# Kernel tuning notes

Measured on AMD Instinct MI355X. Metric: run time of the kernel, lower is better.

The kernel has to match this reference:

```python
import jax, jax.numpy as jnp
import numpy as np

B, T, C, HS = 256, 256, 384, 64

def setup_inputs() -> dict:
    key = jax.random.key(0)
    k1, k2, k3, k4 = jax.random.split(key, 4)
    s = 1.0 / np.sqrt(C)  # Linear-like init scale
    return {
        "x": jax.random.normal(k1, (B, T, C), dtype=jnp.float32),
        "Wq": jax.random.normal(k2, (C, HS), dtype=jnp.float32) * s,
        "Wk": jax.random.normal(k3, (C, HS), dtype=jnp.float32) * s,
        "Wv": jax.random.normal(k4, (C, HS), dtype=jnp.float32) * s,
    }

def reference(x, Wq, Wk, Wv):
    # q,k,v: [B,T,HS]
    q = jnp.einsum("btc,ch->bth", x, Wq)
    k = jnp.einsum("btc,ch->bth", x, Wk)
    v = jnp.einsum("btc,ch->bth", x, Wv)
    scale = k.shape[-1] ** -0.5
    scores = jnp.einsum("bth,bsh->bts", q, k) * scale  # [B,T,T]
    causal = jnp.tril(jnp.ones((x.shape[1], x.shape[1]), dtype=bool))
    scores = jnp.where(causal, scores, -jnp.inf)
    attn = jax.nn.softmax(scores, axis=-1)
    # dropout omitted (eval mode / deterministic reference)
    return jnp.einsum("bts,bsh->bth", attn, v)
```

## Files before the change

kernel.cpp:

```cpp
#include <hip/hip_runtime.h>
#include <hip/hip_bf16.h>

#define NB 256
#define NT 256
#define NC 384
#define NH 64
#define NW 192
#define WT_ELEMS (NW * NC)

typedef short bf16x8 __attribute__((ext_vector_type(8)));
typedef float f32x4 __attribute__((ext_vector_type(4)));

__device__ __forceinline__ unsigned short f2bf(float f) {
  union { float f; unsigned int i; } c;
  c.f = f;
  const unsigned int r = c.i + 0x7fffu + ((c.i >> 16) & 1u);
  return (unsigned short)(r >> 16);
}

__device__ __forceinline__ unsigned short f2bf_hw(float f) {
  __hip_bfloat16 b = __float2bfloat16(f);
  return *reinterpret_cast<unsigned short*>(&b);
}

__device__ __forceinline__ bf16x8 cvt8(float4 lo, float4 hi) {
  union { bf16x8 v; unsigned short u[8]; } au;
  au.u[0] = f2bf_hw(lo.x); au.u[1] = f2bf_hw(lo.y);
  au.u[2] = f2bf_hw(lo.z); au.u[3] = f2bf_hw(lo.w);
  au.u[4] = f2bf_hw(hi.x); au.u[5] = f2bf_hw(hi.y);
  au.u[6] = f2bf_hw(hi.z); au.u[7] = f2bf_hw(hi.w);
  return au.v;
}

__global__ __launch_bounds__(256) void w_prep_kernel(
    const float* __restrict__ Wq,
    const float* __restrict__ Wk,
    const float* __restrict__ Wv,
    unsigned short* __restrict__ Wt2) {
  const int o = blockIdx.x * 256 + threadIdx.x;
  if (o >= WT_ELEMS) return;
  const int j = o & 7;
  const int lane = (o >> 3) & 63;
  const int fi = o >> 9;
  const int ni = fi % 12;
  const int kt = fi / 12;
  const int n = ni * 16 + (lane & 15);
  const int k = kt * 32 + ((lane >> 4) << 3) + j;
  const float* W = (n < 64) ? Wq : (n < 128) ? Wk : Wv;
  Wt2[o] = f2bf(W[k * NH + (n & 63)]);
}

__global__ __launch_bounds__(512, 2) void fused_qkv_attn_kernel(
    const float* __restrict__ x,
    const unsigned short* __restrict__ Wt2,
    float* __restrict__ out) {
  __shared__ __align__(16) unsigned char lds[118784];

  const int tid = threadIdx.x;
  const int w = tid >> 6;
  const int lane = tid & 63;
  const int l15 = lane & 15;
  const int lg = lane >> 4;
  const int b = blockIdx.x;
  const int row0 = b * NT;
  const int qt = (w < 4) ? w : 11 - w;
  const int wbase = qt * 32;

  f32x4 acc[2][12];
#pragma unroll
  for (int mi = 0; mi < 2; ++mi)
#pragma unroll
    for (int ni = 0; ni < 12; ++ni)
#pragma unroll
      for (int r = 0; r < 4; ++r) acc[mi][ni][r] = 0.f;

  const float* xa0 = x + (size_t)(row0 + wbase + l15) * NC + lg * 8;
  const float* xa1 = xa0 + (size_t)16 * NC;
  const unsigned short* wfrag = Wt2 + lane * 8;

#pragma unroll 2
  for (int kt = 0; kt < 12; ++kt) {
    const float4 a0lo = *reinterpret_cast<const float4*>(xa0 + kt * 32);
    const float4 a0hi = *reinterpret_cast<const float4*>(xa0 + kt * 32 + 4);
    const float4 a1lo = *reinterpret_cast<const float4*>(xa1 + kt * 32);
    const float4 a1hi = *reinterpret_cast<const float4*>(xa1 + kt * 32 + 4);
    const bf16x8 afr0 = cvt8(a0lo, a0hi);
    const bf16x8 afr1 = cvt8(a1lo, a1hi);
#pragma unroll
    for (int ni = 0; ni < 12; ++ni) {
      const bf16x8 bfr = *reinterpret_cast<const bf16x8*>(
          wfrag + (size_t)(kt * 12 + ni) * 512);
      acc[0][ni] = __builtin_amdgcn_mfma_f32_16x16x32_bf16(
          afr0, bfr, acc[0][ni], 0, 0, 0);
      acc[1][ni] = __builtin_amdgcn_mfma_f32_16x16x32_bf16(
          afr1, bfr, acc[1][ni], 0, 0, 0);
    }
  }

  unsigned short* Kls = reinterpret_cast<unsigned short*>(lds);
  unsigned short* Vtls = reinterpret_cast<unsigned short*>(lds + 32768);
  unsigned short* Qls = reinterpret_cast<unsigned short*>(lds + 65536);
  unsigned short* Pls = reinterpret_cast<unsigned short*>(lds + 98304);

#pragma unroll
  for (int mi = 0; mi < 2; ++mi)
#pragma unroll
    for (int ni = 0; ni < 12; ++ni) {
      const int n = ni * 16 + l15;
#pragma unroll
      for (int r = 0; r < 4; ++r) {
        const int srow = wbase + mi * 16 + lg * 4 + r;
        const unsigned short val = f2bf_hw(acc[mi][ni][r]);
        if (ni < 4) {
          Qls[srow * 64 + (n ^ ((srow & 7) << 3))] = val;
        } else if (ni < 8) {
          const int h = n - 64;
          Kls[srow * 64 + (h ^ ((srow & 7) << 3))] = val;
        } else {
          const int h = n - 128;
          Vtls[h * 256 + (srow ^ ((h & 7) << 3))] = val;
        }
      }
    }
  __syncthreads();

  const int q0 = wbase;
  bf16x8 a_q[2][2];
#pragma unroll
  for (int mi = 0; mi < 2; ++mi)
#pragma unroll
    for (int ks = 0; ks < 2; ++ks) {
      const int srow = q0 + mi * 16 + l15;
      a_q[mi][ks] = *reinterpret_cast<const bf16x8*>(
          Qls + srow * 64 + ((ks * 32 + lg * 8) ^ ((srow & 7) << 3)));
    }

  f32x4 o[2][4];
  float mrun[2][4], lrun[2][4];
#pragma unroll
  for (int mi = 0; mi < 2; ++mi)
#pragma unroll
    for (int r = 0; r < 4; ++r) {
      mrun[mi][r] = -3.0e38f;
      lrun[mi][r] = 0.f;
#pragma unroll
      for (int hi = 0; hi < 4; ++hi) o[mi][hi][r] = 0.f;
    }

  unsigned short* Pw = Pls + w * 1280;

  for (int j = 0; j <= qt; ++j) {
    f32x4 s_acc[2][2];
#pragma unroll
    for (int mi = 0; mi < 2; ++mi)
#pragma unroll
      for (int si = 0; si < 2; ++si)
#pragma unroll
        for (int r = 0; r < 4; ++r) s_acc[mi][si][r] = 0.f;

#pragma unroll
    for (int ks = 0; ks < 2; ++ks) {
      bf16x8 bk[2];
#pragma unroll
      for (int si = 0; si < 2; ++si) {
        const int srow = j * 32 + si * 16 + l15;
        const int kel = ks * 32 + lg * 8;
        bk[si] = *reinterpret_cast<const bf16x8*>(
            Kls + srow * 64 + (kel ^ ((srow & 7) << 3)));
      }
#pragma unroll
      for (int mi = 0; mi < 2; ++mi)
#pragma unroll
        for (int si = 0; si < 2; ++si)
          s_acc[mi][si] = __builtin_amdgcn_mfma_f32_16x16x32_bf16(
              a_q[mi][ks], bk[si], s_acc[mi][si], 0, 0, 0);
    }

    const bool diag = (j == qt);
#pragma unroll
    for (int mi = 0; mi < 2; ++mi) {
#pragma unroll
      for (int r = 0; r < 4; ++r) {
        const int mloc = mi * 16 + lg * 4 + r;
        float v0 = s_acc[mi][0][r] * 0.125f;
        float v1 = s_acc[mi][1][r] * 0.125f;
        if (diag) {
          if (l15 > mloc) v0 = -3.0e38f;
          if (16 + l15 > mloc) v1 = -3.0e38f;
        }
        float pm = fmaxf(v0, v1);
        pm = fmaxf(pm, __shfl_xor(pm, 1, 16));
        pm = fmaxf(pm, __shfl_xor(pm, 2, 16));
        pm = fmaxf(pm, __shfl_xor(pm, 4, 16));
        pm = fmaxf(pm, __shfl_xor(pm, 8, 16));
        const float mnew = fmaxf(mrun[mi][r], pm);
        const float alpha = __expf(mrun[mi][r] - mnew);
        mrun[mi][r] = mnew;
        const float p0 = __expf(v0 - mnew);
        const float p1 = __expf(v1 - mnew);
        float ps = p0 + p1;
        ps += __shfl_xor(ps, 1, 16);
        ps += __shfl_xor(ps, 2, 16);
        ps += __shfl_xor(ps, 4, 16);
        ps += __shfl_xor(ps, 8, 16);
        lrun[mi][r] = lrun[mi][r] * alpha + ps;
#pragma unroll
        for (int hi = 0; hi < 4; ++hi) o[mi][hi][r] *= alpha;
        Pw[mloc * 40 + l15] = f2bf(p0);
        Pw[mloc * 40 + 16 + l15] = f2bf(p1);
      }
    }

    bf16x8 pa[2];
#pragma unroll
    for (int mt = 0; mt < 2; ++mt)
      pa[mt] = *reinterpret_cast<const bf16x8*>(
          Pw + (mt * 16 + l15) * 40 + lg * 8);
#pragma unroll
    for (int hi = 0; hi < 4; ++hi) {
      const int h = hi * 16 + l15;
      const int sel = j * 32 + lg * 8;
      const bf16x8 bv = *reinterpret_cast<const bf16x8*>(
          Vtls + h * 256 + (sel ^ ((h & 7) << 3)));
#pragma unroll
      for (int mt = 0; mt < 2; ++mt)
        o[mt][hi] = __builtin_amdgcn_mfma_f32_16x16x32_bf16(
            pa[mt], bv, o[mt][hi], 0, 0, 0);
    }
  }

  float* og = out + ((size_t)b * NT + q0) * NH;
#pragma unroll
  for (int mi = 0; mi < 2; ++mi)
#pragma unroll
    for (int r = 0; r < 4; ++r) {
      const float inv = 1.f / lrun[mi][r];
      const int m = mi * 16 + lg * 4 + r;
#pragma unroll
      for (int hi = 0; hi < 4; ++hi)
        og[m * 64 + hi * 16 + l15] = o[mi][hi][r] * inv;
    }
}

extern "C" void kernel_launch(void* const* d_in, const int* in_sizes, int n_in,
                              void* d_out, int out_size, void* d_ws,
                              size_t ws_size, hipStream_t stream) {
  const float* x  = (const float*)d_in[0];
  const float* Wq = (const float*)d_in[1];
  const float* Wk = (const float*)d_in[2];
  const float* Wv = (const float*)d_in[3];
  unsigned short* Wt2 = (unsigned short*)d_ws;
  float* out = (float*)d_out;

  w_prep_kernel<<<dim3((WT_ELEMS + 255) / 256), dim3(256), 0, stream>>>(
      Wq, Wk, Wv, Wt2);
  fused_qkv_attn_kernel<<<dim3(NB), dim3(512), 0, stream>>>(x, Wt2, out);
}
```

Measured before the change: 44.94 us.

## Stage packed weights into LDS via async global_load_lds and prefetch x three deep

The whole packed bf16 weight matrix (144 KB) is now copied into LDS at kernel start with global_load_lds, so the QKV projection reads B fragments from LDS instead of re-reading them from global/L2 in every wave. The x row loads are software-pipelined three k-steps ahead with explicit register buffers and a manual vmcnt wait. The larger LDS footprint (147456 bytes) likely allows only one block per CU instead of two, which reduces occupancy and latency hiding. A barrier is added after the projection before the LDS is reused for Q/K/V.

```diff
diff --git a/kernel.cpp b/kernel.cpp
--- a/kernel.cpp
+++ b/kernel.cpp
@@ -54,7 +54,7 @@
     const float* __restrict__ x,
     const unsigned short* __restrict__ Wt2,
     float* __restrict__ out) {
-  __shared__ __align__(16) unsigned char lds[118784];
+  __shared__ __align__(16) unsigned char lds[147456];
 
   const int tid = threadIdx.x;
   const int w = tid >> 6;
@@ -74,28 +74,58 @@
 #pragma unroll
       for (int r = 0; r < 4; ++r) acc[mi][ni][r] = 0.f;
 
+#pragma unroll
+  for (int i = 0; i < 18; ++i) {
+    const int idx = i * 512 + tid;
+    __builtin_amdgcn_global_load_lds(
+        (const __attribute__((address_space(1))) void*)(Wt2 + idx * 8),
+        (__attribute__((address_space(3))) void*)(lds + idx * 16), 16, 0, 0);
+  }
+
   const float* xa0 = x + (size_t)(row0 + wbase + l15) * NC + lg * 8;
   const float* xa1 = xa0 + (size_t)16 * NC;
-  const unsigned short* wfrag = Wt2 + lane * 8;
-
-#pragma unroll 2
-  for (int kt = 0; kt < 12; ++kt) {
-    const float4 a0lo = *reinterpret_cast<const float4*>(xa0 + kt * 32);
-    const float4 a0hi = *reinterpret_cast<const float4*>(xa0 + kt * 32 + 4);
-    const float4 a1lo = *reinterpret_cast<const float4*>(xa1 + kt * 32);
-    const float4 a1hi = *reinterpret_cast<const float4*>(xa1 + kt * 32 + 4);
-    const bf16x8 afr0 = cvt8(a0lo, a0hi);
-    const bf16x8 afr1 = cvt8(a1lo, a1hi);
-#pragma unroll
-    for (int ni = 0; ni < 12; ++ni) {
-      const bf16x8 bfr = *reinterpret_cast<const bf16x8*>(
-          wfrag + (size_t)(kt * 12 + ni) * 512);
-      acc[0][ni] = __builtin_amdgcn_mfma_f32_16x16x32_bf16(
-          afr0, bfr, acc[0][ni], 0, 0, 0);
-      acc[1][ni] = __builtin_amdgcn_mfma_f32_16x16x32_bf16(
-          afr1, bfr, acc[1][ni], 0, 0, 0);
-    }
-  }
+
+  float4 aA0, aA1, aA2, aA3, aB0, aB1, aB2, aB3, aC0, aC1, aC2, aC3;
+
+#define LOADA(S, KT)                                                          \
+  do {                                                                        \
+    a##S##0 = *reinterpret_cast<const float4*>(xa0 + (KT)*32);                \
+    a##S##1 = *reinterpret_cast<const float4*>(xa0 + (KT)*32 + 4);            \
+    a##S##2 = *reinterpret_cast<const float4*>(xa1 + (KT)*32);                \
+    a##S##3 = *reinterpret_cast<const float4*>(xa1 + (KT)*32 + 4);            \
+  } while (0)
+
+  LOADA(A, 0);
+  LOADA(B, 1);
+  LOADA(C, 2);
+
+  asm volatile("s_waitcnt vmcnt(12)" ::: "memory");
+  __builtin_amdgcn_s_barrier();
+
+  const unsigned short* Wl =
+      reinterpret_cast<const unsigned short*>(lds) + lane * 8;
+
+#define STEP(S, KT)                                                           \
+  do {                                                                        \
+    const bf16x8 afr0 = cvt8(a##S##0, a##S##1);                               \
+    const bf16x8 afr1 = cvt8(a##S##2, a##S##3);                               \
+    if ((KT) + 3 < 12) LOADA(S, (KT) + 3);                                    \
+    _Pragma("unroll") for (int ni = 0; ni < 12; ++ni) {                       \
+      const bf16x8 bfr = *reinterpret_cast<const bf16x8*>(                    \
+          Wl + (size_t)((KT)*12 + ni) * 512);                                 \
+      acc[0][ni] = __builtin_amdgcn_mfma_f32_16x16x32_bf16(                   \
+          afr0, bfr, acc[0][ni], 0, 0, 0);                                    \
+      acc[1][ni] = __builtin_amdgcn_mfma_f32_16x16x32_bf16(                   \
+          afr1, bfr, acc[1][ni], 0, 0, 0);                                    \
+    }                                                                         \
+  } while (0)
+
+  STEP(A, 0);  STEP(B, 1);  STEP(C, 2);
+  STEP(A, 3);  STEP(B, 4);  STEP(C, 5);
+  STEP(A, 6);  STEP(B, 7);  STEP(C, 8);
+  STEP(A, 9);  STEP(B, 10); STEP(C, 11);
+
+  __syncthreads();
 
   unsigned short* Kls = reinterpret_cast<unsigned short*>(lds);
   unsigned short* Vtls = reinterpret_cast<unsigned short*>(lds + 32768);
```

New measurement: 44.22 us. No clear change (-1.6%).

## Stage x and weights through LDS with async global_load_lds double buffering

Applied to the files above, without the earlier changes.

Rewrites the QKV projection so weight fragments are copied into LDS in three K-thirds using async global_load_lds with two buffers. x tiles are loaded coalesced, converted to bf16 and stored swizzled into per-wave LDS regions, with manual waitcnt and barriers used to overlap loads with MFMA work. This removes redundant per-wave global weight reads and uncoalesced x loads. In exchange LDS grows to 160KB, which likely limits occupancy to one block per CU, and the hand-written vmcnt counts are fragile.

```diff
diff --git a/kernel.cpp b/kernel.cpp
--- a/kernel.cpp
+++ b/kernel.cpp
@@ -21,15 +21,6 @@
 __device__ __forceinline__ unsigned short f2bf_hw(float f) {
   __hip_bfloat16 b = __float2bfloat16(f);
   return *reinterpret_cast<unsigned short*>(&b);
-}
-
-__device__ __forceinline__ bf16x8 cvt8(float4 lo, float4 hi) {
-  union { bf16x8 v; unsigned short u[8]; } au;
-  au.u[0] = f2bf_hw(lo.x); au.u[1] = f2bf_hw(lo.y);
-  au.u[2] = f2bf_hw(lo.z); au.u[3] = f2bf_hw(lo.w);
-  au.u[4] = f2bf_hw(hi.x); au.u[5] = f2bf_hw(hi.y);
-  au.u[6] = f2bf_hw(hi.z); au.u[7] = f2bf_hw(hi.w);
-  return au.v;
 }
 
 __global__ __launch_bounds__(256) void w_prep_kernel(
@@ -54,7 +45,7 @@
     const float* __restrict__ x,
     const unsigned short* __restrict__ Wt2,
     float* __restrict__ out) {
-  __shared__ __align__(16) unsigned char lds[118784];
+  __shared__ __align__(16) unsigned char lds[163840];
 
   const int tid = threadIdx.x;
   const int w = tid >> 6;
@@ -74,28 +65,89 @@
 #pragma unroll
       for (int r = 0; r < 4; ++r) acc[mi][ni][r] = 0.f;
 
-  const float* xa0 = x + (size_t)(row0 + wbase + l15) * NC + lg * 8;
-  const float* xa1 = xa0 + (size_t)16 * NC;
-  const unsigned short* wfrag = Wt2 + lane * 8;
-
-#pragma unroll 2
-  for (int kt = 0; kt < 12; ++kt) {
-    const float4 a0lo = *reinterpret_cast<const float4*>(xa0 + kt * 32);
-    const float4 a0hi = *reinterpret_cast<const float4*>(xa0 + kt * 32 + 4);
-    const float4 a1lo = *reinterpret_cast<const float4*>(xa1 + kt * 32);
-    const float4 a1hi = *reinterpret_cast<const float4*>(xa1 + kt * 32 + 4);
-    const bf16x8 afr0 = cvt8(a0lo, a0hi);
-    const bf16x8 afr1 = cvt8(a1lo, a1hi);
-#pragma unroll
-    for (int ni = 0; ni < 12; ++ni) {
-      const bf16x8 bfr = *reinterpret_cast<const bf16x8*>(
-          wfrag + (size_t)(kt * 12 + ni) * 512);
-      acc[0][ni] = __builtin_amdgcn_mfma_f32_16x16x32_bf16(
-          afr0, bfr, acc[0][ni], 0, 0, 0);
-      acc[1][ni] = __builtin_amdgcn_mfma_f32_16x16x32_bf16(
-          afr1, bfr, acc[1][ni], 0, 0, 0);
-    }
-  }
+  float4 xr[16];
+
+#define XLOAD(T)                                                              \
+  {                                                                           \
+    _Pragma("unroll") for (int i = 0; i < 16; ++i) {                          \
+      const int idx_ = i * 64 + lane;                                         \
+      const int r_ = idx_ >> 5, c_ = idx_ & 31;                               \
+      xr[i] = *reinterpret_cast<const float4*>(                               \
+          x + (size_t)(row0 + wbase + r_) * NC + (T)*128 + c_ * 4);           \
+    }                                                                         \
+  }
+
+#define XWRITE()                                                              \
+  {                                                                           \
+    _Pragma("unroll") for (int i = 0; i < 16; ++i) {                          \
+      const int idx_ = i * 64 + lane;                                         \
+      const int r_ = idx_ >> 5, c_ = idx_ & 31;                               \
+      ushort4 t_;                                                             \
+      t_.x = f2bf_hw(xr[i].x); t_.y = f2bf_hw(xr[i].y);                       \
+      t_.z = f2bf_hw(xr[i].z); t_.w = f2bf_hw(xr[i].w);                       \
+      *reinterpret_cast<ushort4*>(lds + w * 8192 + (r_ >> 4) * 4096 +         \
+                                  (r_ & 15) * 256 +                           \
+                                  ((((c_ >> 1) ^ (r_ & 7)) << 4)) +           \
+                                  (c_ & 1) * 8) = t_;                         \
+    }                                                                         \
+  }
+
+#define WSTAGE(BUF, T)                                                        \
+  {                                                                           \
+    _Pragma("unroll") for (int j = 0; j < 6; ++j) {                           \
+      const int ch_ = j * 512 + tid;                                          \
+      __builtin_amdgcn_global_load_lds(                                       \
+          (const __attribute__((address_space(1))) void*)(Wt2 + (T)*24576 +   \
+                                                          ch_ * 8),           \
+          (__attribute__((address_space(3))) void*)(lds + 65536 +             \
+                                                    (BUF)*49152 + ch_ * 16),  \
+          16, 0, 0);                                                          \
+    }                                                                         \
+  }
+
+#define CTHIRD(BUF)                                                           \
+  {                                                                           \
+    _Pragma("unroll") for (int kl = 0; kl < 4; ++kl) {                        \
+      const int ch_ = ((kl * 4 + lg) ^ (l15 & 7)) << 4;                       \
+      const bf16x8 af0 = *reinterpret_cast<const bf16x8*>(                    \
+          lds + w * 8192 + l15 * 256 + ch_);                                  \
+      const bf16x8 af1 = *reinterpret_cast<const bf16x8*>(                    \
+          lds + w * 8192 + 4096 + l15 * 256 + ch_);                           \
+      _Pragma("unroll") for (int ni = 0; ni < 12; ++ni) {                     \
+        const bf16x8 bfr = *reinterpret_cast<const bf16x8*>(                  \
+            lds + 65536 + (BUF)*49152 + (kl * 12 + ni) * 1024 + lane * 16);   \
+        acc[0][ni] = __builtin_amdgcn_mfma_f32_16x16x32_bf16(                 \
+            af0, bfr, acc[0][ni], 0, 0, 0);                                   \
+        acc[1][ni] = __builtin_amdgcn_mfma_f32_16x16x32_bf16(                 \
+            af1, bfr, acc[1][ni], 0, 0, 0);                                   \
+      }                                                                       \
+    }                                                                         \
+  }
+
+  XLOAD(0);
+  WSTAGE(0, 0);
+  WSTAGE(1, 1);
+  asm volatile("s_waitcnt vmcnt(12)" ::: "memory");
+  XWRITE();
+  XLOAD(1);
+  asm volatile("s_waitcnt vmcnt(16)" ::: "memory");
+  asm volatile("s_waitcnt lgkmcnt(0)" ::: "memory");
+  __builtin_amdgcn_s_barrier();
+  CTHIRD(0);
+  __builtin_amdgcn_s_barrier();
+  WSTAGE(0, 2);
+  asm volatile("s_waitcnt vmcnt(6)" ::: "memory");
+  XWRITE();
+  XLOAD(2);
+  asm volatile("s_waitcnt lgkmcnt(0)" ::: "memory");
+  CTHIRD(1);
+  asm volatile("s_waitcnt vmcnt(0)" ::: "memory");
+  XWRITE();
+  asm volatile("s_waitcnt lgkmcnt(0)" ::: "memory");
+  __builtin_amdgcn_s_barrier();
+  CTHIRD(0);
+
+  __syncthreads();
 
   unsigned short* Kls = reinterpret_cast<unsigned short*>(lds);
   unsigned short* Vtls = reinterpret_cast<unsigned short*>(lds + 32768);
```

Measured after the change: 54.35 us. 20.9% more time.
